# Optimization experiments

Measured on AMD Instinct MI355X. Metric: run time of the kernel, lower is better.

## Reference

```python
import math
import jax, jax.numpy as jnp
import numpy as np

B, N, D = 16, 4096, 256
N_CAT, N_TPC, N_VPT, N_SP = 16, 8, 4, 16
N_TYPE = N_CAT * N_TPC          # 128
N_VAR = N_TYPE * N_VPT          # 512
THRESH = 0.1
MASK_VAL = jnp.finfo(jnp.float32).min / 2


def _linear(x, w, b):
    # torch nn.Linear: y = x @ W^T + b, W: (out, in)
    return x @ w.T + b


def _level(codes, proj_w, proj_b, K, X, mask, tau):
    """One codebook level: attention of codes over tokens.
    codes: (M, d). Returns H:(B,M,d), w_raw:(B,M)."""
    Q = _linear(codes, proj_w, proj_b)                       # (M, d)
    attn = jnp.einsum('md,bnd->bmn', Q, K) / math.sqrt(D)    # (B, M, N)
    attn = jnp.where(mask[:, None, :], attn, MASK_VAL)
    attn = jnp.clip(attn, -50.0, 50.0)
    G = jnp.nan_to_num(jax.nn.softmax(attn, axis=-1))        # (B, M, N)
    H = jnp.einsum('bmn,bnd->bmd', G, X)                     # (B, M, d)
    w_raw = jnp.linalg.norm(H, axis=-1) / tau                # (B, M)
    return H, w_raw


def _sparsify(w, thr):
    ws = jnp.where(w > thr, w, 0.0)
    return ws / (ws.sum(axis=-1, keepdims=True) + 1e-8)


def _forward(X, positions, category_codes, type_codes, variant_codes,
             spatial_codes, log_tau, cat_w, cat_b, type_w, type_b,
             var_w, var_b, sp_w, sp_b, k_w, k_b, g1_w, g1_b, g2_w, g2_b,
             out_w, out_b, ln_g, ln_b, level_weights, mask):
    tau = jnp.clip(jnp.exp(log_tau[0]) + 0.1, 0.1, 2.0)
    K = _linear(X, k_w, k_b)                                 # (B, N, d)

    # Level 0: category
    H_cat, w_cat_raw = _level(category_codes, cat_w, cat_b, K, X, mask, tau)
    w_cat = jax.nn.softmax(w_cat_raw, axis=-1)
    w_cat_sp = _sparsify(w_cat, THRESH)

    # Level 1: type, gated by category selection
    H_type, w_type_raw = _level(type_codes.reshape(-1, D), type_w, type_b,
                                K, X, mask, tau)
    w_t = (w_type_raw.reshape(-1, N_CAT, N_TPC) * w_cat_sp[:, :, None]
           ).reshape(-1, N_TYPE)
    w_type = jax.nn.softmax(w_t, axis=-1)
    w_type_sp = _sparsify(w_type, THRESH / 2)

    # Level 2: variant, gated by type selection
    H_var, w_var_raw = _level(variant_codes.reshape(-1, D), var_w, var_b,
                              K, X, mask, tau)
    w_type_exp = jnp.repeat(w_type_sp, N_VPT, axis=-1)       # (B, 512)
    w_var = jax.nn.softmax(w_var_raw * w_type_exp, axis=-1)
    w_var_sp = _sparsify(w_var, THRESH / 4)

    # Spatial level (independent)
    H_sp, w_sp_raw = _level(spatial_codes, sp_w, sp_b, K, X, mask, tau)
    w_sp = jax.nn.softmax(w_sp_raw, axis=-1)
    w_sp_sp = _sparsify(w_sp, THRESH)

    z_cat = jnp.einsum('bm,bmd->bd', w_cat_sp, H_cat)
    z_type = jnp.einsum('bm,bmd->bd', w_type_sp, H_type)
    z_var = jnp.einsum('bm,bmd->bd', w_var_sp, H_var)
    z_spatial = jnp.einsum('bm,bmd->bd', w_sp_sp, H_sp)

    # Position gating of category summary
    mask_f = mask.astype(X.dtype)[:, :, None]
    pos_pooled = (positions * mask_f).sum(1) / jnp.maximum(mask_f.sum(1), 1.0)
    gate_in = jnp.concatenate([z_cat, pos_pooled], axis=-1)  # (B, 2d)
    h = jax.nn.gelu(_linear(gate_in, g1_w, g1_b), approximate=False)
    pos_gate = jax.nn.sigmoid(_linear(h, g2_w, g2_b))
    z_cat = z_cat * pos_gate

    # Learned level combine + gated output projection
    lw = jax.nn.softmax(level_weights)
    z = (lw[0] * z_cat + lw[1] * z_type + lw[2] * z_var + lw[3] * z_spatial)
    z = _linear(z, out_w, out_b)
    mu = z.mean(-1, keepdims=True)
    var = z.var(-1, keepdims=True)
    z = (z - mu) / jnp.sqrt(var + 1e-5) * ln_g + ln_b
    return z


def setup_inputs() -> dict:
    key = jax.random.key(0)
    ks = jax.random.split(key, 32)
    s = 1.0 / math.sqrt(D)
    inp = {
        'X': jax.random.normal(ks[0], (B, N, D), jnp.float32),
        'positions': jax.random.normal(ks[1], (B, N, D), jnp.float32),
        'category_codes': jax.random.normal(ks[2], (N_CAT, D)) * 0.02,
        'type_codes': jax.random.normal(ks[3], (N_CAT, N_TPC, D)) * 0.02,
        'variant_codes': jax.random.normal(ks[4], (N_CAT, N_TPC, N_VPT, D)) * 0.02,
        'spatial_codes': jax.random.normal(ks[5], (N_SP, D)) * 0.02,
        'log_tau': jnp.zeros((1,), jnp.float32),
        'cat_w': jax.random.normal(ks[6], (D, D)) * s,
        'cat_b': jnp.zeros((D,)),
        'type_w': jax.random.normal(ks[7], (D, D)) * s,
        'type_b': jnp.zeros((D,)),
        'var_w': jax.random.normal(ks[8], (D, D)) * s,
        'var_b': jnp.zeros((D,)),
        'sp_w': jax.random.normal(ks[9], (D, D)) * s,
        'sp_b': jnp.zeros((D,)),
        'k_w': jax.random.normal(ks[10], (D, D)) * s,
        'k_b': jnp.zeros((D,)),
        'g1_w': jax.random.normal(ks[11], (D, 2 * D)) * s,
        'g1_b': jnp.zeros((D,)),
        'g2_w': jax.random.normal(ks[12], (D, D)) * s,
        'g2_b': jnp.zeros((D,)),
        'out_w': jax.random.normal(ks[13], (D, D)) * s,
        'out_b': jnp.zeros((D,)),
        'ln_g': jnp.ones((D,)),
        'ln_b': jnp.zeros((D,)),
        'level_weights': jnp.ones((4,)) / 4.0,
        'mask': jnp.ones((B, N), jnp.bool_),
    }
    return inp


def reference(X, positions, category_codes, type_codes, variant_codes,
              spatial_codes, log_tau, cat_w, cat_b, type_w, type_b,
              var_w, var_b, sp_w, sp_b, k_w, k_b, g1_w, g1_b, g2_w, g2_b,
              out_w, out_b, ln_g, ln_b, level_weights, mask):
    return _forward(X, positions, category_codes, type_codes, variant_codes,
                    spatial_codes, log_tau, cat_w, cat_b, type_w, type_b,
                    var_w, var_b, sp_w, sp_b, k_w, k_b, g1_w, g1_b,
                    g2_w, g2_b, out_w, out_b, ln_g, ln_b, level_weights, mask)
```

## Files before the change

kernel.cpp:

```cpp
#include <hip/hip_runtime.h>


#define DEV static __device__ __forceinline__

typedef short bf16x8 __attribute__((ext_vector_type(8)));
typedef float f32x4 __attribute__((ext_vector_type(4)));
typedef unsigned short u16x8 __attribute__((ext_vector_type(8)));

DEV float bf2f(unsigned short u) {
  return __uint_as_float(((unsigned int)u) << 16);
}
DEV unsigned short f2bf(float f) {
  unsigned int x = __float_as_uint(f);
  unsigned int r = (x + 0x7fffu + ((x >> 16) & 1u)) >> 16;
  return (unsigned short)r;
}

DEV void gl2lds16(const void* g, void* l) {
  __builtin_amdgcn_global_load_lds(
      (const __attribute__((address_space(1))) unsigned int*)g,
      (__attribute__((address_space(3))) unsigned int*)l, 16, 0, 0);
}

DEV bf16x8 pack8(const float4 a, const float4 b) {
  bf16x8 r;
  r[0] = (short)f2bf(a.x); r[1] = (short)f2bf(a.y);
  r[2] = (short)f2bf(a.z); r[3] = (short)f2bf(a.w);
  r[4] = (short)f2bf(b.x); r[5] = (short)f2bf(b.y);
  r[6] = (short)f2bf(b.z); r[7] = (short)f2bf(b.w);
  return r;
}

DEV size_t pk_off(int rt, int ks) { return ((size_t)rt * 8 + ks) * 512; }

__global__ __launch_bounds__(256) void kproj_mfma(
    const float* __restrict__ X, const float* __restrict__ W,
    const float* __restrict__ bias, unsigned short* __restrict__ Kp) {
  __shared__ __align__(16) unsigned short As[128 * 72];
  __shared__ __align__(16) unsigned short Bs[128 * 72];
  const int m0 = blockIdx.x * 128, c0 = blockIdx.y * 128;
  const int t = threadIdx.x, l = t & 63, w = t >> 6;
  const int wm = (w & 1) * 64, wn = (w >> 1) * 64;
  const f32x4 zero = {0.f, 0.f, 0.f, 0.f};
  f32x4 acc[4][4];
#pragma unroll
  for (int i = 0; i < 4; ++i)
#pragma unroll
    for (int j = 0; j < 4; ++j) acc[i][j] = zero;
  const int rr = t >> 3, cc = (t & 7) * 8;
  for (int kc = 0; kc < 256; kc += 64) {
    __syncthreads();
#pragma unroll
    for (int p = 0; p < 4; ++p) {
      const int r = p * 32 + rr;
      const float* xs = &X[(size_t)(m0 + r) * 256 + kc + cc];
      const float4 a0 = *(const float4*)&xs[0];
      const float4 a1 = *(const float4*)&xs[4];
      *(bf16x8*)&As[r * 72 + cc] = pack8(a0, a1);
      const float* wsrc = &W[(size_t)(c0 + r) * 256 + kc + cc];
      const float4 b0 = *(const float4*)&wsrc[0];
      const float4 b1 = *(const float4*)&wsrc[4];
      *(bf16x8*)&Bs[r * 72 + cc] = pack8(b0, b1);
    }
    __syncthreads();
#pragma unroll
    for (int ks = 0; ks < 2; ++ks) {
      const int koff = ks * 32 + ((l >> 4) & 3) * 8;
      bf16x8 a[4], b[4];
#pragma unroll
      for (int f = 0; f < 4; ++f)
        a[f] = *(const bf16x8*)&As[(wm + f * 16 + (l & 15)) * 72 + koff];
#pragma unroll
      for (int f = 0; f < 4; ++f)
        b[f] = *(const bf16x8*)&Bs[(wn + f * 16 + (l & 15)) * 72 + koff];
#pragma unroll
      for (int i = 0; i < 4; ++i)
#pragma unroll
        for (int j = 0; j < 4; ++j)
          acc[i][j] =
              __builtin_amdgcn_mfma_f32_16x16x32_bf16(a[i], b[j], acc[i][j],
                                                      0, 0, 0);
    }
  }
  const int q = (l >> 4) & 3;
#pragma unroll
  for (int j = 0; j < 4; ++j) {
    const int c = c0 + wn + j * 16 + (l & 15);
    const float bv = bias[c];
#pragma unroll
    for (int i = 0; i < 4; ++i) {
      const int mrow = m0 + wm + i * 16 + q * 4;
#pragma unroll
      for (int r = 0; r < 4; ++r) {
        const int m = mrow + r;
        Kp[pk_off(m >> 4, c >> 5) + ((m & 15) + 16 * ((c >> 3) & 3)) * 8 +
           (c & 7)] = f2bf(acc[i][j][r] + bv);
      }
    }
  }
}

__global__ __launch_bounds__(256) void xT_kern(const float* __restrict__ X,
                                               unsigned short* __restrict__ XTp) {
  __shared__ float Ls[64][65];
  const int tn = blockIdx.x, td = blockIdx.y, b = blockIdx.z;
  const int t = threadIdx.x;
  const int nl = t >> 2, dp = (t & 3) * 16;
  const float* src =
      X + ((size_t)b * 4096 + tn * 64 + nl) * 256 + td * 64 + dp;
#pragma unroll
  for (int v = 0; v < 4; ++v) {
    const float4 x = *(const float4*)&src[v * 4];
    Ls[nl][dp + v * 4 + 0] = x.x;
    Ls[nl][dp + v * 4 + 1] = x.y;
    Ls[nl][dp + v * 4 + 2] = x.z;
    Ls[nl][dp + v * 4 + 3] = x.w;
  }
  __syncthreads();
  const int dl = t >> 2, np = (t & 3) * 16;
  u16x8 h0, h1;
#pragma unroll
  for (int j = 0; j < 8; ++j) h0[j] = f2bf(Ls[np + j][dl]);
#pragma unroll
  for (int j = 0; j < 8; ++j) h1[j] = f2bf(Ls[np + 8 + j][dl]);
  const int d = td * 64 + dl;
  const int n0g = tn * 64 + np;
  const int n1g = n0g + 8;
  unsigned short* dst = XTp + (size_t)b * 1048576;
  const size_t o0 = (((size_t)(d >> 4) * 128) + (n0g >> 5)) * 512 +
                    ((d & 15) + 16 * ((n0g >> 3) & 3)) * 8;
  const size_t o1 = (((size_t)(d >> 4) * 128) + (n1g >> 5)) * 512 +
                    ((d & 15) + 16 * ((n1g >> 3) & 3)) * 8;
  *(u16x8*)&dst[o0] = h0;
  *(u16x8*)&dst[o1] = h1;
}

__global__ __launch_bounds__(256) void qproj_kern(
    const float* __restrict__ cat_codes, const float* __restrict__ type_codes,
    const float* __restrict__ var_codes, const float* __restrict__ sp_codes,
    const float* __restrict__ cat_w, const float* __restrict__ cat_b,
    const float* __restrict__ type_w, const float* __restrict__ type_b,
    const float* __restrict__ var_w, const float* __restrict__ var_b,
    const float* __restrict__ sp_w, const float* __restrict__ sp_b,
    unsigned short* __restrict__ Qp) {
  const int m = blockIdx.x;
  const int t = threadIdx.x;
  const size_t off = pk_off(m >> 4, t >> 5) +
                     ((m & 15) + 16 * ((t >> 3) & 3)) * 8 + (t & 7);
  if (m >= 672) {
    Qp[off] = 0;
    return;
  }
  const float* code;
  const float* W;
  const float* bias;
  if (m < 16)       { code = cat_codes  + m * 256;         W = cat_w;  bias = cat_b; }
  else if (m < 144) { code = type_codes + (m - 16) * 256;  W = type_w; bias = type_b; }
  else if (m < 656) { code = var_codes  + (m - 144) * 256; W = var_w;  bias = var_b; }
  else              { code = sp_codes   + (m - 656) * 256; W = sp_w;   bias = sp_b; }
  __shared__ float xs[256];
  xs[t] = code[t];
  __syncthreads();
  float a = bias[t];
  const float* wr = W + (size_t)t * 256;
  for (int k = 0; k < 256; k += 4) {
    const float4 w = *(const float4*)&wr[k];
    a = fmaf(w.x, xs[k], a);
    a = fmaf(w.y, xs[k + 1], a);
    a = fmaf(w.z, xs[k + 2], a);
    a = fmaf(w.w, xs[k + 3], a);
  }
  Qp[off] = f2bf(a);
}

__global__ __launch_bounds__(256, 2) void attn_fused(
    const unsigned short* __restrict__ Qp, const unsigned short* __restrict__ Kp,
    const unsigned short* __restrict__ XTp,
    const unsigned char* __restrict__ mask, float* __restrict__ H,
    float* __restrict__ lsum) {
  __shared__ __align__(16) unsigned short Ks[2][16384];
  __shared__ __align__(16) unsigned short Plds[64 * 72];
  __shared__ unsigned char msk[1024];
  const int combo = blockIdx.x;
  const int m0 = blockIdx.y * 64;
  const int b = combo >> 2;
  const int nbase = (combo & 3) * 1024;
  const int t = threadIdx.x, l = t & 63, w = t >> 6;
  const int l15 = l & 15, q = l >> 4;
  ((uchar4*)msk)[t] = ((const uchar4*)(mask + (size_t)b * 4096 + nbase))[t];
  const int mt_g = (m0 >> 4) + w;
  bf16x8 qf[8];
#pragma unroll
  for (int ks = 0; ks < 8; ++ks)
    qf[ks] = *(const bf16x8*)&Qp[pk_off(mt_g, ks) + l * 8];
  const f32x4 zero = {0.f, 0.f, 0.f, 0.f};
  f32x4 accO[4][4];
#pragma unroll
  for (int i = 0; i < 4; ++i)
#pragma unroll
    for (int j = 0; j < 4; ++j) accO[i][j] = zero;
  f32x4 rs = zero;
  const unsigned short* XTb = XTp + (size_t)b * 1048576;
  const unsigned short* Kchunk0 = Kp + ((size_t)b * 256 + (nbase >> 4)) * 4096;
#pragma unroll
  for (int i = 0; i < 8; ++i)
    gl2lds16(Kchunk0 + (w * 8 + i) * 512 + l * 8, &Ks[0][(w * 8 + i) * 512]);
  for (int c = 0; c < 16; ++c) {
    const int cur = c & 1;
    __syncthreads();
    const int nst0 = (nbase >> 5) + c * 2;
    bf16x8 xf[2][4];
#pragma unroll
    for (int ks2 = 0; ks2 < 2; ++ks2)
#pragma unroll
      for (int dj = 0; dj < 4; ++dj)
        xf[ks2][dj] = *(const bf16x8*)&XTb[((size_t)(4 * w + dj) * 128 +
                                            nst0 + ks2) * 512 + l * 8];
    f32x4 accS[4];
#pragma unroll
    for (int f = 0; f < 4; ++f) accS[f] = zero;
#pragma unroll
    for (int ks = 0; ks < 8; ++ks) {
      bf16x8 kf[4];
#pragma unroll
      for (int f = 0; f < 4; ++f)
        kf[f] = *(const bf16x8*)&Ks[cur][(f * 8 + ks) * 512 + l * 8];
#pragma unroll
      for (int f = 0; f < 4; ++f)
        accS[f] = __builtin_amdgcn_mfma_f32_16x16x32_bf16(qf[ks], kf[f],
                                                          accS[f], 0, 0, 0);
    }
#pragma unroll
    for (int f = 0; f < 4; ++f) {
      const bool mk = msk[c * 64 + f * 16 + l15] != 0;
#pragma unroll
      for (int r = 0; r < 4; ++r) {
        float s = accS[f][r] * 0.0625f;
        s = fminf(fmaxf(s, -50.f), 50.f);
        if (!mk) s = -50.f;
        const float e = __expf(s);
        Plds[(w * 16 + q * 4 + r) * 72 + f * 16 + l15] = f2bf(e);
        rs[r] += e;
      }
    }
    __syncthreads();
    if (c < 15) {
      const unsigned short* src = Kchunk0 + (size_t)(c + 1) * 16384;
      unsigned short* dst = &Ks[1 - cur][0];
#pragma unroll
      for (int i = 0; i < 8; ++i)
        gl2lds16(src + (w * 8 + i) * 512 + l * 8, dst + (w * 8 + i) * 512);
    }
#pragma unroll
    for (int ks2 = 0; ks2 < 2; ++ks2) {
      bf16x8 pf[4];
#pragma unroll
      for (int mt = 0; mt < 4; ++mt)
        pf[mt] = *(const bf16x8*)&Plds[(mt * 16 + l15) * 72 + ks2 * 32 + q * 8];
#pragma unroll
      for (int mt = 0; mt < 4; ++mt)
#pragma unroll
        for (int dj = 0; dj < 4; ++dj)
          accO[mt][dj] = __builtin_amdgcn_mfma_f32_16x16x32_bf16(
              pf[mt], xf[ks2][dj], accO[mt][dj], 0, 0, 0);
    }
  }
#pragma unroll
  for (int r = 0; r < 4; ++r) {
    float v = rs[r];
    v += __shfl_xor(v, 1, 64);
    v += __shfl_xor(v, 2, 64);
    v += __shfl_xor(v, 4, 64);
    v += __shfl_xor(v, 8, 64);
    const int m = m0 + w * 16 + q * 4 + r;
    if (l15 == 0 && m < 672) atomicAdd(&lsum[b * 672 + m], v);
  }
#pragma unroll
  for (int mt = 0; mt < 4; ++mt) {
    const int mbase = m0 + mt * 16 + q * 4;
#pragma unroll
    for (int dj = 0; dj < 4; ++dj) {
      const int d = w * 64 + dj * 16 + l15;
#pragma unroll
      for (int r = 0; r < 4; ++r) {
        const int m = mbase + r;
        if (m < 672)
          atomicAdd(&H[((size_t)b * 672 + m) * 256 + d], accO[mt][dj][r]);
      }
    }
  }
}

__global__ __launch_bounds__(256) void hnorm_kern(
    const float* __restrict__ H, const float* __restrict__ lsum,
    const float* __restrict__ log_tau, float* __restrict__ wraw) {
  const int b = blockIdx.x, j = blockIdx.y;
  const int t = threadIdx.x, l = t & 63, w = t >> 6;
  const int m = j * 4 + w;
  const float4 v = *(const float4*)&H[((size_t)b * 672 + m) * 256 + l * 4];
  float ss = v.x * v.x + v.y * v.y + v.z * v.z + v.w * v.w;
#pragma unroll
  for (int s = 1; s < 64; s <<= 1) ss += __shfl_xor(ss, s, 64);
  if (l == 0) {
    const float tau = fminf(fmaxf(expf(log_tau[0]) + 0.1f, 0.1f), 2.0f);
    wraw[b * 672 + m] = sqrtf(ss) / (lsum[b * 672 + m] * tau);
  }
}

__global__ __launch_bounds__(256) void pospool_kern(
    const float* __restrict__ pos, const unsigned char* __restrict__ mask,
    float* __restrict__ pacc, float* __restrict__ cnt) {
  const int b = blockIdx.x, seg = blockIdx.y, t = threadIdx.x;
  const int dg = t & 63;
  const int nl = t >> 6;
  const int n0 = seg * 128;
  float4 acc = make_float4(0.f, 0.f, 0.f, 0.f);
  float c = 0.f;
  const float* pb = pos + (size_t)b * 4096 * 256;
  for (int j = 0; j < 32; ++j) {
    const int n = n0 + j * 4 + nl;
    const float mf = mask[(size_t)b * 4096 + n] ? 1.f : 0.f;
    const float4 v = *(const float4*)&pb[(size_t)n * 256 + dg * 4];
    acc.x = fmaf(mf, v.x, acc.x);
    acc.y = fmaf(mf, v.y, acc.y);
    acc.z = fmaf(mf, v.z, acc.z);
    acc.w = fmaf(mf, v.w, acc.w);
    c += mf;
  }
  __shared__ float4 red4[256];
  __shared__ float redc[4];
  red4[t] = acc;
  if (dg == 0) redc[nl] = c;
  __syncthreads();
  if (t < 64) {
    float4 s = red4[t];
    const float4 s1 = red4[t + 64], s2 = red4[t + 128], s3 = red4[t + 192];
    s.x += s1.x + s2.x + s3.x;
    s.y += s1.y + s2.y + s3.y;
    s.z += s1.z + s2.z + s3.z;
    s.w += s1.w + s2.w + s3.w;
    float* pa = pacc + b * 256 + t * 4;
    atomicAdd(pa + 0, s.x);
    atomicAdd(pa + 1, s.y);
    atomicAdd(pa + 2, s.z);
    atomicAdd(pa + 3, s.w);
    if (t == 0) atomicAdd(&cnt[b], redc[0] + redc[1] + redc[2] + redc[3]);
  }
}

DEV float wave_max(float v) {
#pragma unroll
  for (int m = 1; m < 64; m <<= 1) v = fmaxf(v, __shfl_xor(v, m, 64));
  return v;
}
DEV float wave_sum(float v) {
#pragma unroll
  for (int m = 1; m < 64; m <<= 1) v += __shfl_xor(v, m, 64);
  return v;
}

__global__ __launch_bounds__(256) void combine_kern(
    const float* __restrict__ wraw, const float* __restrict__ lsum,
    const float* __restrict__ H, float* __restrict__ zbuf) {
  const int b = blockIdx.x, j = blockIdx.y, t = threadIdx.x, l = t & 63;
  __shared__ float wr[672];
  __shared__ float wsp[672];
  for (int i = t; i < 672; i += 256) wr[i] = wraw[b * 672 + i];
  __syncthreads();
  {
    const float v = (l < 16) ? wr[l] : -1e30f;
    const float mx = wave_max(v);
    const float e = (l < 16) ? expf(wr[l] - mx) : 0.f;
    const float s = wave_sum(e);
    float w = e / s;
    w = (w > 0.1f) ? w : 0.f;
    const float s2 = wave_sum(w);
    if (l < 16) wsp[l] = w / (s2 + 1e-8f);
  }
  __syncthreads();
  {
    const float L0 = wr[16 + l] * wsp[l >> 3];
    const float L1 = wr[16 + 64 + l] * wsp[(64 + l) >> 3];
    const float mx = wave_max(fmaxf(L0, L1));
    const float e0 = expf(L0 - mx), e1 = expf(L1 - mx);
    const float s = wave_sum(e0 + e1);
    float w0 = e0 / s, w1 = e1 / s;
    w0 = (w0 > 0.05f) ? w0 : 0.f;
    w1 = (w1 > 0.05f) ? w1 : 0.f;
    const float s2 = wave_sum(w0 + w1);
    const float inv2 = 1.f / (s2 + 1e-8f);
    wsp[16 + l] = w0 * inv2;
    wsp[16 + 64 + l] = w1 * inv2;
  }
  __syncthreads();
  {
    float Lv[8];
    float lm = -1e30f;
#pragma unroll
    for (int jj = 0; jj < 8; ++jj) {
      const int i = l * 8 + jj;
      Lv[jj] = wr[144 + i] * wsp[16 + (i >> 2)];
      lm = fmaxf(lm, Lv[jj]);
    }
    const float mx = wave_max(lm);
    float ls = 0.f;
#pragma unroll
    for (int jj = 0; jj < 8; ++jj) {
      Lv[jj] = expf(Lv[jj] - mx);
      ls += Lv[jj];
    }
    const float s = wave_sum(ls);
    const float inv = 1.f / s;
    float ls2 = 0.f;
#pragma unroll
    for (int jj = 0; jj < 8; ++jj) {
      float w = Lv[jj] * inv;
      w = (w > 0.025f) ? w : 0.f;
      Lv[jj] = w;
      ls2 += w;
    }
    const float s2 = wave_sum(ls2);
    const float inv2 = 1.f / (s2 + 1e-8f);
#pragma unroll
    for (int jj = 0; jj < 8; ++jj) wsp[144 + l * 8 + jj] = Lv[jj] * inv2;
  }
  __syncthreads();
  {
    const float v = (l < 16) ? wr[656 + l] : -1e30f;
    const float mx = wave_max(v);
    const float e = (l < 16) ? expf(wr[656 + l] - mx) : 0.f;
    const float s = wave_sum(e);
    float w = e / s;
    w = (w > 0.1f) ? w : 0.f;
    const float s2 = wave_sum(w);
    if (l < 16) wsp[656 + l] = w / (s2 + 1e-8f);
  }
  __syncthreads();
  for (int i = t; i < 672; i += 256) wsp[i] = wsp[i] / lsum[b * 672 + i];
  __syncthreads();
  const float* Hb = H + (size_t)b * 672 * 256 + t;
  const int s0 = j * 84, s1 = s0 + 84;
  const int Llo[4] = {0, 16, 144, 656};
  const int Lhi[4] = {16, 144, 656, 672};
#pragma unroll
  for (int lv = 0; lv < 4; ++lv) {
    const int lo = max(s0, Llo[lv]);
    const int hi = min(s1, Lhi[lv]);
    if (lo >= hi) continue;
    float z = 0.f;
    for (int m = lo; m < hi; ++m)
      z = fmaf(wsp[m], Hb[(size_t)m * 256], z);
    atomicAdd(&zbuf[(b * 4 + lv) * 256 + t], z);
  }
}

__global__ __launch_bounds__(256) void gate_kern(
    const float* __restrict__ zbuf, const float* __restrict__ pacc,
    const float* __restrict__ cnt, const float* __restrict__ g1_w,
    const float* __restrict__ g1_b, const float* __restrict__ g2_w,
    const float* __restrict__ g2_b, const float* __restrict__ out_w,
    const float* __restrict__ out_b, const float* __restrict__ ln_g,
    const float* __restrict__ ln_b, const float* __restrict__ lvlw,
    float* __restrict__ out) {
  const int b = blockIdx.x, t = threadIdx.x;
  __shared__ float gin[512];
  __shared__ float hb[256];
  __shared__ float zc[256];
  __shared__ float red[256];
  const float z0 = zbuf[(b * 4 + 0) * 256 + t];
  gin[t] = z0;
  const float c = fmaxf(cnt[b], 1.0f);
  gin[256 + t] = pacc[b * 256 + t] / c;
  __syncthreads();
  float a = g1_b[t];
  const float* w1 = g1_w + (size_t)t * 512;
  for (int k = 0; k < 512; k += 4) {
    const float4 w = *(const float4*)&w1[k];
    a = fmaf(w.x, gin[k], a);
    a = fmaf(w.y, gin[k + 1], a);
    a = fmaf(w.z, gin[k + 2], a);
    a = fmaf(w.w, gin[k + 3], a);
  }
  const float hg = 0.5f * a * (1.0f + erff(a * 0.7071067811865475f));
  hb[t] = hg;
  __syncthreads();
  float a2 = g2_b[t];
  const float* w2 = g2_w + (size_t)t * 256;
  for (int k = 0; k < 256; k += 4) {
    const float4 w = *(const float4*)&w2[k];
    a2 = fmaf(w.x, hb[k], a2);
    a2 = fmaf(w.y, hb[k + 1], a2);
    a2 = fmaf(w.z, hb[k + 2], a2);
    a2 = fmaf(w.w, hb[k + 3], a2);
  }
  const float pg = 1.0f / (1.0f + expf(-a2));
  const float l0 = lvlw[0], l1 = lvlw[1], l2 = lvlw[2], l3 = lvlw[3];
  const float mx = fmaxf(fmaxf(l0, l1), fmaxf(l2, l3));
  const float e0 = expf(l0 - mx), e1 = expf(l1 - mx);
  const float e2 = expf(l2 - mx), e3 = expf(l3 - mx);
  const float einv = 1.0f / (e0 + e1 + e2 + e3);
  const float zmix = (e0 * z0 * pg + e1 * zbuf[(b * 4 + 1) * 256 + t] +
                      e2 * zbuf[(b * 4 + 2) * 256 + t] +
                      e3 * zbuf[(b * 4 + 3) * 256 + t]) * einv;
  zc[t] = zmix;
  __syncthreads();
  float o = out_b[t];
  const float* wo = out_w + (size_t)t * 256;
  for (int k = 0; k < 256; k += 4) {
    const float4 w = *(const float4*)&wo[k];
    o = fmaf(w.x, zc[k], o);
    o = fmaf(w.y, zc[k + 1], o);
    o = fmaf(w.z, zc[k + 2], o);
    o = fmaf(w.w, zc[k + 3], o);
  }
  red[t] = o;
  __syncthreads();
  for (int s = 128; s > 0; s >>= 1) {
    if (t < s) red[t] += red[t + s];
    __syncthreads();
  }
  const float mu = red[0] / 256.f;
  __syncthreads();
  red[t] = o * o;
  __syncthreads();
  for (int s = 128; s > 0; s >>= 1) {
    if (t < s) red[t] += red[t + s];
    __syncthreads();
  }
  const float var = red[0] / 256.f - mu * mu;
  out[b * 256 + t] = (o - mu) * rsqrtf(var + 1e-5f) * ln_g[t] + ln_b[t];
}

extern "C" void kernel_launch(void* const* d_in, const int* in_sizes, int n_in,
                              void* d_out, int out_size, void* d_ws,
                              size_t ws_size, hipStream_t stream) {
  (void)in_sizes; (void)n_in; (void)out_size; (void)ws_size;
  const float* X          = (const float*)d_in[0];
  const float* positions  = (const float*)d_in[1];
  const float* cat_codes  = (const float*)d_in[2];
  const float* type_codes = (const float*)d_in[3];
  const float* var_codes  = (const float*)d_in[4];
  const float* sp_codes   = (const float*)d_in[5];
  const float* log_tau    = (const float*)d_in[6];
  const float* cat_w      = (const float*)d_in[7];
  const float* cat_b      = (const float*)d_in[8];
  const float* type_w     = (const float*)d_in[9];
  const float* type_b     = (const float*)d_in[10];
  const float* var_w      = (const float*)d_in[11];
  const float* var_b      = (const float*)d_in[12];
  const float* sp_w       = (const float*)d_in[13];
  const float* sp_b       = (const float*)d_in[14];
  const float* k_w        = (const float*)d_in[15];
  const float* k_b        = (const float*)d_in[16];
  const float* g1_w       = (const float*)d_in[17];
  const float* g1_b       = (const float*)d_in[18];
  const float* g2_w       = (const float*)d_in[19];
  const float* g2_b       = (const float*)d_in[20];
  const float* out_w      = (const float*)d_in[21];
  const float* out_b      = (const float*)d_in[22];
  const float* ln_g       = (const float*)d_in[23];
  const float* ln_b       = (const float*)d_in[24];
  const float* lvlw       = (const float*)d_in[25];
  const unsigned char* mask = (const unsigned char*)d_in[26];

  char* ws = (char*)d_ws;
  constexpr size_t O_KP  = 0;
  constexpr size_t O_XT  = 33554432;
  constexpr size_t O_QP  = 67108864;
  constexpr size_t O_H   = 67469312;
  constexpr size_t O_L   = 78479360;
  constexpr size_t O_WR  = 78522368;
  constexpr size_t O_PA  = 78565376;
  constexpr size_t O_CNT = 78581760;
  constexpr size_t O_Z   = 78581824;

  unsigned short* Kp  = (unsigned short*)(ws + O_KP);
  unsigned short* XTp = (unsigned short*)(ws + O_XT);
  unsigned short* Qp  = (unsigned short*)(ws + O_QP);
  float* H            = (float*)(ws + O_H);
  float* lsum         = (float*)(ws + O_L);
  float* wraw         = (float*)(ws + O_WR);
  float* pacc         = (float*)(ws + O_PA);
  float* cnt          = (float*)(ws + O_CNT);
  float* zbuf         = (float*)(ws + O_Z);
  float* out          = (float*)d_out;

  hipMemsetAsync(lsum, 0, 16 * 672 * 4, stream);
  hipMemsetAsync(H, 0, 11010048, stream);
  hipMemsetAsync(pacc, 0, 16 * 256 * 4, stream);
  hipMemsetAsync(cnt, 0, 64, stream);
  hipMemsetAsync(zbuf, 0, 16 * 4 * 256 * 4, stream);

  qproj_kern<<<dim3(704), 256, 0, stream>>>(
      cat_codes, type_codes, var_codes, sp_codes, cat_w, cat_b, type_w, type_b,
      var_w, var_b, sp_w, sp_b, Qp);
  kproj_mfma<<<dim3(512, 2), 256, 0, stream>>>(X, k_w, k_b, Kp);
  xT_kern<<<dim3(64, 4, 16), 256, 0, stream>>>(X, XTp);
  pospool_kern<<<dim3(16, 32), 256, 0, stream>>>(positions, mask, pacc, cnt);

  attn_fused<<<dim3(64, 11), 256, 0, stream>>>(Qp, Kp, XTp, mask, H, lsum);

  hnorm_kern<<<dim3(16, 168), 256, 0, stream>>>(H, lsum, log_tau, wraw);
  combine_kern<<<dim3(16, 8), 256, 0, stream>>>(wraw, lsum, H, zbuf);
  gate_kern<<<dim3(16), 256, 0, stream>>>(zbuf, pacc, cnt, g1_w, g1_b, g2_w,
                                          g2_b, out_w, out_b, ln_g, ln_b, lvlw,
                                          out);
}
```

Measured before the change: 424.8 us.

## Split attention over two N halves with plain partial stores instead of atomics

```diff
diff --git a/kernel.cpp b/kernel.cpp
--- a/kernel.cpp
+++ b/kernel.cpp
@@ -176,18 +176,19 @@
 __global__ __launch_bounds__(256, 2) void attn_fused(
     const unsigned short* __restrict__ Qp, const unsigned short* __restrict__ Kp,
     const unsigned short* __restrict__ XTp,
-    const unsigned char* __restrict__ mask, float* __restrict__ H,
-    float* __restrict__ lsum) {
+    const unsigned char* __restrict__ mask, float* __restrict__ H2,
+    float* __restrict__ lsum2) {
   __shared__ __align__(16) unsigned short Ks[2][16384];
   __shared__ __align__(16) unsigned short Plds[64 * 72];
-  __shared__ unsigned char msk[1024];
+  __shared__ unsigned char msk[2048];
   const int combo = blockIdx.x;
   const int m0 = blockIdx.y * 64;
-  const int b = combo >> 2;
-  const int nbase = (combo & 3) * 1024;
+  const int b = combo >> 1;
+  const int nsl = combo & 1;
+  const int nbase = nsl * 2048;
   const int t = threadIdx.x, l = t & 63, w = t >> 6;
   const int l15 = l & 15, q = l >> 4;
-  ((uchar4*)msk)[t] = ((const uchar4*)(mask + (size_t)b * 4096 + nbase))[t];
+  ((uint2*)msk)[t] = ((const uint2*)(mask + (size_t)b * 4096 + nbase))[t];
   const int mt_g = (m0 >> 4) + w;
   bf16x8 qf[8];
 #pragma unroll
@@ -205,7 +206,7 @@
 #pragma unroll
   for (int i = 0; i < 8; ++i)
     gl2lds16(Kchunk0 + (w * 8 + i) * 512 + l * 8, &Ks[0][(w * 8 + i) * 512]);
-  for (int c = 0; c < 16; ++c) {
+  for (int c = 0; c < 32; ++c) {
     const int cur = c & 1;
     __syncthreads();
     const int nst0 = (nbase >> 5) + c * 2;
@@ -244,7 +245,7 @@
       }
     }
     __syncthreads();
-    if (c < 15) {
+    if (c < 31) {
       const unsigned short* src = Kchunk0 + (size_t)(c + 1) * 16384;
       unsigned short* dst = &Ks[1 - cur][0];
 #pragma unroll
@@ -265,6 +266,7 @@
               pf[mt], xf[ks2][dj], accO[mt][dj], 0, 0, 0);
     }
   }
+  float* lpart = lsum2 + (size_t)(nsl * 16 + b) * 672;
 #pragma unroll
   for (int r = 0; r < 4; ++r) {
     float v = rs[r];
@@ -273,8 +275,9 @@
     v += __shfl_xor(v, 4, 64);
     v += __shfl_xor(v, 8, 64);
     const int m = m0 + w * 16 + q * 4 + r;
-    if (l15 == 0 && m < 672) atomicAdd(&lsum[b * 672 + m], v);
-  }
+    if (l15 == 0 && m < 672) lpart[m] = v;
+  }
+  float* Hpart = H2 + (size_t)(nsl * 16 + b) * 672 * 256;
 #pragma unroll
   for (int mt = 0; mt < 4; ++mt) {
     const int mbase = m0 + mt * 16 + q * 4;
@@ -284,26 +287,35 @@
 #pragma unroll
       for (int r = 0; r < 4; ++r) {
         const int m = mbase + r;
-        if (m < 672)
-          atomicAdd(&H[((size_t)b * 672 + m) * 256 + d], accO[mt][dj][r]);
+        if (m < 672) Hpart[(size_t)m * 256 + d] = accO[mt][dj][r];
       }
     }
   }
 }
 
 __global__ __launch_bounds__(256) void hnorm_kern(
-    const float* __restrict__ H, const float* __restrict__ lsum,
-    const float* __restrict__ log_tau, float* __restrict__ wraw) {
+    const float* __restrict__ H2, const float* __restrict__ lsum2,
+    const float* __restrict__ log_tau, float* __restrict__ H,
+    float* __restrict__ lsum, float* __restrict__ wraw) {
   const int b = blockIdx.x, j = blockIdx.y;
   const int t = threadIdx.x, l = t & 63, w = t >> 6;
   const int m = j * 4 + w;
-  const float4 v = *(const float4*)&H[((size_t)b * 672 + m) * 256 + l * 4];
+  const size_t r0 = ((size_t)b * 672 + m) * 256;
+  const size_t r1 = ((size_t)(16 + b) * 672 + m) * 256;
+  const float4 v0 = *(const float4*)&H2[r0 + l * 4];
+  const float4 v1 = *(const float4*)&H2[r1 + l * 4];
+  float4 v;
+  v.x = v0.x + v1.x; v.y = v0.y + v1.y;
+  v.z = v0.z + v1.z; v.w = v0.w + v1.w;
+  *(float4*)&H[r0 + l * 4] = v;
   float ss = v.x * v.x + v.y * v.y + v.z * v.z + v.w * v.w;
 #pragma unroll
   for (int s = 1; s < 64; s <<= 1) ss += __shfl_xor(ss, s, 64);
   if (l == 0) {
+    const float lt = lsum2[b * 672 + m] + lsum2[(16 + b) * 672 + m];
     const float tau = fminf(fmaxf(expf(log_tau[0]) + 0.1f, 0.1f), 2.0f);
-    wraw[b * 672 + m] = sqrtf(ss) / (lsum[b * 672 + m] * tau);
+    lsum[b * 672 + m] = lt;
+    wraw[b * 672 + m] = sqrtf(ss) / (lt * tau);
   }
 }
 
@@ -567,17 +579,20 @@
   constexpr size_t O_KP  = 0;
   constexpr size_t O_XT  = 33554432;
   constexpr size_t O_QP  = 67108864;
-  constexpr size_t O_H   = 67469312;
-  constexpr size_t O_L   = 78479360;
-  constexpr size_t O_WR  = 78522368;
-  constexpr size_t O_PA  = 78565376;
-  constexpr size_t O_CNT = 78581760;
-  constexpr size_t O_Z   = 78581824;
+  constexpr size_t O_H2  = 67469312;
+  constexpr size_t O_L2  = 89489408;
+  constexpr size_t O_L   = 89575424;
+  constexpr size_t O_WR  = 89618432;
+  constexpr size_t O_PA  = 89661440;
+  constexpr size_t O_CNT = 89677824;
+  constexpr size_t O_Z   = 89677888;
 
   unsigned short* Kp  = (unsigned short*)(ws + O_KP);
   unsigned short* XTp = (unsigned short*)(ws + O_XT);
   unsigned short* Qp  = (unsigned short*)(ws + O_QP);
-  float* H            = (float*)(ws + O_H);
+  float* H2           = (float*)(ws + O_H2);
+  float* H            = (float*)(ws + O_KP);
+  float* lsum2        = (float*)(ws + O_L2);
   float* lsum         = (float*)(ws + O_L);
   float* wraw         = (float*)(ws + O_WR);
   float* pacc         = (float*)(ws + O_PA);
@@ -585,8 +600,6 @@
   float* zbuf         = (float*)(ws + O_Z);
   float* out          = (float*)d_out;
 
-  hipMemsetAsync(lsum, 0, 16 * 672 * 4, stream);
-  hipMemsetAsync(H, 0, 11010048, stream);
   hipMemsetAsync(pacc, 0, 16 * 256 * 4, stream);
   hipMemsetAsync(cnt, 0, 64, stream);
   hipMemsetAsync(zbuf, 0, 16 * 4 * 256 * 4, stream);
@@ -598,9 +611,10 @@
   xT_kern<<<dim3(64, 4, 16), 256, 0, stream>>>(X, XTp);
   pospool_kern<<<dim3(16, 32), 256, 0, stream>>>(positions, mask, pacc, cnt);
 
-  attn_fused<<<dim3(64, 11), 256, 0, stream>>>(Qp, Kp, XTp, mask, H, lsum);
-
-  hnorm_kern<<<dim3(16, 168), 256, 0, stream>>>(H, lsum, log_tau, wraw);
+  attn_fused<<<dim3(32, 11), 256, 0, stream>>>(Qp, Kp, XTp, mask, H2, lsum2);
+
+  hnorm_kern<<<dim3(16, 168), 256, 0, stream>>>(H2, lsum2, log_tau, H, lsum,
+                                                wraw);
   combine_kern<<<dim3(16, 8), 256, 0, stream>>>(wraw, lsum, H, zbuf);
   gate_kern<<<dim3(16), 256, 0, stream>>>(zbuf, pacc, cnt, g1_w, g1_b, g2_w,
                                           g2_b, out_w, out_b, ln_g, ln_b, lvlw,
```

Result: faster. 412.9 us (-2.8%).
